# Kernel optimization log

Measured on AMD Instinct MI355X. Metric: run time of the kernel, lower is better.

Reference implementation:

```python
import jax, jax.numpy as jnp
import numpy as np

N_LAYERS = 8   # internal layers (roots are layer 0)
M = 8192       # nodes per layer
K = 8          # parents per internal node
C = 1 << K     # 256 CPT configurations per node


def setup_inputs() -> dict:
    key = jax.random.key(0)
    k1, k2, k3 = jax.random.split(key, 3)
    # root nodes have 0 parents -> a single logit each (configs_per_node == 1)
    root_logits = jax.random.normal(k1, (M,), dtype=jnp.float32)
    # internal nodes: CPT logits over all 2^K parent configurations
    cpt_logits = jax.random.normal(k2, (N_LAYERS, M, C), dtype=jnp.float32)
    # parents[l, m, j] = index (into previous layer's M nodes) of the j-th parent
    parents = jax.random.randint(k3, (N_LAYERS, M, K), 0, M)
    return {"root_logits": root_logits, "cpt_logits": cpt_logits, "parents": parents}


def reference(root_logits, cpt_logits, parents):
    temp = 1.0
    Kp = parents.shape[-1]
    Cn = cpt_logits.shape[-1]
    # configs matrix, MSB-first, matching _configs_matrix: [C, K]
    bits = ((jnp.arange(Cn)[:, None] >> jnp.arange(Kp - 1, -1, -1)[None, :]) & 1).astype(jnp.float32)

    prev0 = jax.nn.sigmoid(root_logits / temp)  # root marginals: p = sigmoid(logit)

    def step(prev, layer):
        logits_l, par_l = layer
        p = prev[par_l]  # gather parent marginals: [M, K]
        # P(config c | parents) = prod_j (c_j * p_j + (1 - c_j) * (1 - p_j))
        pg = bits[None, :, :] * p[:, None, :] + (1.0 - bits[None, :, :]) * (1.0 - p[:, None, :])  # [M, C, K]
        prod_probs = jnp.prod(pg, axis=-1)  # [M, C]
        p_cpt = jax.nn.sigmoid(logits_l / temp)  # [M, C]
        marg = jnp.einsum('mc,mc->m', p_cpt, prod_probs)  # [M]
        return marg, marg

    _, ys = jax.lax.scan(step, prev0, (cpt_logits, parents))
    # marginals for all nodes in topological (layer) order: [(N_LAYERS+1)*M]
    return jnp.concatenate([prev0[None, :], ys], axis=0).reshape(-1)
```

## Files before the change

kernel.cpp:

```cpp
#include <hip/hip_runtime.h>

#define M_NODES 8192
#define K_PAR 8
#define C_CFG 256
#define N_LAYERS 8
#define TPB 1024
#define NBLOCKS 256
#define WPB (TPB / 64)
#define NPB (WPB * 2)

__device__ __forceinline__ float fsig(float x) {
    return __builtin_amdgcn_rcpf(1.0f + __expf(-x));
}

__device__ __forceinline__ float aloadf(const float* p) {
    return __hip_atomic_load(p, __ATOMIC_RELAXED, __HIP_MEMORY_SCOPE_AGENT);
}
__device__ __forceinline__ void astoref(float* p, float v) {
    __hip_atomic_store(p, v, __ATOMIC_RELAXED, __HIP_MEMORY_SCOPE_AGENT);
}

__global__ __launch_bounds__(TPB, 4) void bayes_flow3(
    const float* root_logits,
    const float* cpt,
    const int*   parents,
    float*       out)
{
    const int tid   = threadIdx.x;
    const int lane  = tid & 63;
    const int b     = blockIdx.x;
    const int gwave = b * WPB + (tid >> 6);
    const int mA    = gwave << 1;
    const int mB    = mA | 1;
    const int c0    = lane << 2;

    float rl = 0.0f;
    if (tid < NPB) rl = root_logits[b * NPB + tid];

    int pidx[N_LAYERS];
    if (lane < 2 * K_PAR) {
        const int node = (lane < K_PAR) ? mA : mB;
#pragma unroll
        for (int l = 0; l < N_LAYERS; ++l)
            pidx[l] = parents[((size_t)l * M_NODES + node) * K_PAR + (lane & 7)];
    }

    float4 qAc = *reinterpret_cast<const float4*>(cpt + (size_t)mA * C_CFG + c0);
    float4 qBc = *reinterpret_cast<const float4*>(cpt + (size_t)mB * C_CFG + c0);

    if (tid < NPB) astoref(out + b * NPB + tid, fsig(rl));

    const float* prev = out;
    float*       cur  = out + M_NODES;

#pragma unroll
    for (int l = 0; l < N_LAYERS; ++l) {
        float4 qAn = {0, 0, 0, 0}, qBn = {0, 0, 0, 0};
        if (l + 1 < N_LAYERS) {
            qAn = *reinterpret_cast<const float4*>(cpt + ((size_t)(l + 1) * M_NODES + mA) * C_CFG + c0);
            qBn = *reinterpret_cast<const float4*>(cpt + ((size_t)(l + 1) * M_NODES + mB) * C_CFG + c0);
        }

        float pv = 1.0f;
        if (lane < 2 * K_PAR) {
            const float* ap = prev + pidx[l];
            pv = aloadf(ap);
            while (!(pv > 0.0f)) { __builtin_amdgcn_s_sleep(1); pv = aloadf(ap); }
        }

        float pAv[K_PAR], pBv[K_PAR];
#pragma unroll
        for (int j = 0; j < K_PAR; ++j) {
            pAv[j] = __shfl(pv, j, 64);
            pBv[j] = __shfl(pv, K_PAR + j, 64);
        }

        float prefA = 1.0f, prefB = 1.0f;
#pragma unroll
        for (int j = 0; j < 6; ++j) {
            const int bit = (c0 >> (7 - j)) & 1;
            prefA *= bit ? pAv[j] : (1.0f - pAv[j]);
            prefB *= bit ? pBv[j] : (1.0f - pBv[j]);
        }
        const float p6A = pAv[6], p7A = pAv[7], q6A = 1.0f - p6A, q7A = 1.0f - p7A;
        const float p6B = pBv[6], p7B = pBv[7], q6B = 1.0f - p6B, q7B = 1.0f - p7B;

        float sA = fsig(qAc.x) * (prefA * q6A * q7A)
                 + fsig(qAc.y) * (prefA * q6A * p7A)
                 + fsig(qAc.z) * (prefA * p6A * q7A)
                 + fsig(qAc.w) * (prefA * p6A * p7A);
        float sB = fsig(qBc.x) * (prefB * q6B * q7B)
                 + fsig(qBc.y) * (prefB * q6B * p7B)
                 + fsig(qBc.z) * (prefB * p6B * q7B)
                 + fsig(qBc.w) * (prefB * p6B * p7B);

#pragma unroll
        for (int off = 32; off; off >>= 1) {
            sA += __shfl_xor(sA, off, 64);
            sB += __shfl_xor(sB, off, 64);
        }
        if (lane == 0) {
            astoref(cur + mA, sA);
            astoref(cur + mB, sB);
        }

        qAc = qAn; qBc = qBn;
        asm volatile("" : "+v"(qAc.x), "+v"(qAc.y), "+v"(qAc.z), "+v"(qAc.w),
                          "+v"(qBc.x), "+v"(qBc.y), "+v"(qBc.z), "+v"(qBc.w));

        prev = cur;
        cur += M_NODES;
    }
}

extern "C" void kernel_launch(void* const* d_in, const int* in_sizes, int n_in,
                              void* d_out, int out_size, void* d_ws, size_t ws_size,
                              hipStream_t stream) {
    const float* root_logits = (const float*)d_in[0];
    const float* cpt_logits  = (const float*)d_in[1];
    const int*   parents     = (const int*)d_in[2];
    float*       out         = (float*)d_out;

    bayes_flow3<<<NBLOCKS, TPB, 0, stream>>>(root_logits, cpt_logits, parents, out);
}
```

Before: 128.5 us.

## Add sharded per-layer ready counters as a grid-wide gate before parent polling

Adds a workspace array of per-layer, per-shard ready counters. Each block increments its shard counter after writing its layer outputs, and one wave per block spins until all eight shards reach the target before the block reads parent values. This is meant to replace scattered per-value polling on the output array with a cheaper barrier-like gate that cuts cache-line contention. The sigmoids are also hoisted ahead of the wait and the two outputs are written with one 64-bit store. In exchange it adds an extra init kernel launch, two __syncthreads per layer and a bounded spin that could hang or time out if blocks are not all co-resident.

```diff
diff --git a/kernel.cpp b/kernel.cpp
--- a/kernel.cpp
+++ b/kernel.cpp
@@ -8,23 +8,39 @@
 #define NBLOCKS 256
 #define WPB (TPB / 64)
 #define NPB (WPB * 2)
+#define NSHARD 8
+#define SHARD_STRIDE 16
+#define GATE_TARGET 1024u
+#define RDY_WORDS ((N_LAYERS + 1) * NSHARD * SHARD_STRIDE)
 
 __device__ __forceinline__ float fsig(float x) {
     return __builtin_amdgcn_rcpf(1.0f + __expf(-x));
 }
-
 __device__ __forceinline__ float aloadf(const float* p) {
+    return __hip_atomic_load(p, __ATOMIC_RELAXED, __HIP_MEMORY_SCOPE_AGENT);
+}
+__device__ __forceinline__ unsigned aloadu(const unsigned* p) {
     return __hip_atomic_load(p, __ATOMIC_RELAXED, __HIP_MEMORY_SCOPE_AGENT);
 }
 __device__ __forceinline__ void astoref(float* p, float v) {
     __hip_atomic_store(p, v, __ATOMIC_RELAXED, __HIP_MEMORY_SCOPE_AGENT);
 }
+__device__ __forceinline__ void astore2(float* p, float lo, float hi) {
+    union { float f[2]; unsigned long long u; } v;
+    v.f[0] = lo; v.f[1] = hi;
+    __hip_atomic_store((unsigned long long*)p, v.u, __ATOMIC_RELAXED, __HIP_MEMORY_SCOPE_AGENT);
+}
 
-__global__ __launch_bounds__(TPB, 4) void bayes_flow3(
+__global__ __launch_bounds__(256) void init_rdy(unsigned* rdy) {
+    for (int i = threadIdx.x; i < RDY_WORDS; i += 256) rdy[i] = 0u;
+}
+
+__global__ __launch_bounds__(TPB, 4) void bayes_flow5(
     const float* root_logits,
     const float* cpt,
     const int*   parents,
-    float*       out)
+    float*       out,
+    unsigned*    rdy)
 {
     const int tid   = threadIdx.x;
     const int lane  = tid & 63;
@@ -33,6 +49,7 @@
     const int mA    = gwave << 1;
     const int mB    = mA | 1;
     const int c0    = lane << 2;
+    const int shard = b >> 5;
 
     float rl = 0.0f;
     if (tid < NPB) rl = root_logits[b * NPB + tid];
@@ -49,6 +66,10 @@
     float4 qBc = *reinterpret_cast<const float4*>(cpt + (size_t)mB * C_CFG + c0);
 
     if (tid < NPB) astoref(out + b * NPB + tid, fsig(rl));
+    __syncthreads();
+    if (tid == 0)
+        __hip_atomic_fetch_add(rdy + shard * SHARD_STRIDE, 32u,
+                               __ATOMIC_RELAXED, __HIP_MEMORY_SCOPE_AGENT);
 
     const float* prev = out;
     float*       cur  = out + M_NODES;
@@ -61,11 +82,26 @@
             qBn = *reinterpret_cast<const float4*>(cpt + ((size_t)(l + 1) * M_NODES + mB) * C_CFG + c0);
         }
 
+        const float sA0 = fsig(qAc.x), sA1 = fsig(qAc.y), sA2 = fsig(qAc.z), sA3 = fsig(qAc.w);
+        const float sB0 = fsig(qBc.x), sB1 = fsig(qBc.y), sB2 = fsig(qBc.z), sB3 = fsig(qBc.w);
+
+        if (tid < 64) {
+            const unsigned* base = rdy + (size_t)l * NSHARD * SHARD_STRIDE;
+            int budget = 1 << 22;
+            for (;;) {
+                bool ok = true;
+                if (lane < NSHARD) ok = (aloadu(base + lane * SHARD_STRIDE) >= GATE_TARGET);
+                if (__all(ok) || --budget <= 0) break;
+                __builtin_amdgcn_s_sleep(1);
+            }
+        }
+        __syncthreads();
+
         float pv = 1.0f;
         if (lane < 2 * K_PAR) {
             const float* ap = prev + pidx[l];
             pv = aloadf(ap);
-            while (!(pv > 0.0f)) { __builtin_amdgcn_s_sleep(1); pv = aloadf(ap); }
+            while (!(pv > 0.0f)) { __builtin_amdgcn_s_sleep(2); pv = aloadf(ap); }
         }
 
         float pAv[K_PAR], pBv[K_PAR];
@@ -85,23 +121,24 @@
         const float p6A = pAv[6], p7A = pAv[7], q6A = 1.0f - p6A, q7A = 1.0f - p7A;
         const float p6B = pBv[6], p7B = pBv[7], q6B = 1.0f - p6B, q7B = 1.0f - p7B;
 
-        float sA = fsig(qAc.x) * (prefA * q6A * q7A)
-                 + fsig(qAc.y) * (prefA * q6A * p7A)
-                 + fsig(qAc.z) * (prefA * p6A * q7A)
-                 + fsig(qAc.w) * (prefA * p6A * p7A);
-        float sB = fsig(qBc.x) * (prefB * q6B * q7B)
-                 + fsig(qBc.y) * (prefB * q6B * p7B)
-                 + fsig(qBc.z) * (prefB * p6B * q7B)
-                 + fsig(qBc.w) * (prefB * p6B * p7B);
+        float sA = sA0 * (prefA * q6A * q7A) + sA1 * (prefA * q6A * p7A)
+                 + sA2 * (prefA * p6A * q7A) + sA3 * (prefA * p6A * p7A);
+        float sB = sB0 * (prefB * q6B * q7B) + sB1 * (prefB * q6B * p7B)
+                 + sB2 * (prefB * p6B * q7B) + sB3 * (prefB * p6B * p7B);
 
 #pragma unroll
         for (int off = 32; off; off >>= 1) {
             sA += __shfl_xor(sA, off, 64);
             sB += __shfl_xor(sB, off, 64);
         }
-        if (lane == 0) {
-            astoref(cur + mA, sA);
-            astoref(cur + mB, sB);
+        if (lane == 0) astore2(cur + mA, sA, sB);
+
+        if (l + 1 < N_LAYERS) {
+            __syncthreads();
+            if (tid == 0)
+                __hip_atomic_fetch_add(rdy + (size_t)(l + 1) * NSHARD * SHARD_STRIDE
+                                           + shard * SHARD_STRIDE, 32u,
+                                       __ATOMIC_RELAXED, __HIP_MEMORY_SCOPE_AGENT);
         }
 
         qAc = qAn; qBc = qBn;
@@ -120,6 +157,8 @@
     const float* cpt_logits  = (const float*)d_in[1];
     const int*   parents     = (const int*)d_in[2];
     float*       out         = (float*)d_out;
+    unsigned*    rdy         = (unsigned*)d_ws;
 
-    bayes_flow3<<<NBLOCKS, TPB, 0, stream>>>(root_logits, cpt_logits, parents, out);
+    init_rdy<<<1, 256, 0, stream>>>(rdy);
+    bayes_flow5<<<NBLOCKS, TPB, 0, stream>>>(root_logits, cpt_logits, parents, out, rdy);
 }
```

After: 115.0 us. 1.12x faster.
